# Performance work log

Measured on AMD Instinct MI355X. Metric: run time of the kernel, lower is better.

Reference implementation:

```python
import jax, jax.numpy as jnp
import numpy as np

D_MODEL, H, D_FF = 512, 8, 2048
DK = D_MODEL // H
EPS = 1e-5  # torch LayerNorm default


def layer_norm(x, g, b):
    m = jnp.mean(x, axis=-1, keepdims=True)
    v = jnp.mean((x - m) ** 2, axis=-1, keepdims=True)
    return (x - m) * jax.lax.rsqrt(v + EPS) * g + b


def setup_inputs() -> dict:
    key = jax.random.key(0)
    ks = jax.random.split(key, 10)
    B, S = 8, 2048
    s = lambda fan_in: 1.0 / np.sqrt(fan_in)
    return {
        "x": jax.random.normal(ks[0], (B, S, D_MODEL), jnp.float32),
        # per-head projections stacked: [h, d_model, dk] (bias-free Project)
        "wq": jax.random.uniform(ks[1], (H, D_MODEL, DK), jnp.float32, -s(D_MODEL), s(D_MODEL)),
        "wk": jax.random.uniform(ks[2], (H, D_MODEL, DK), jnp.float32, -s(D_MODEL), s(D_MODEL)),
        "wv": jax.random.uniform(ks[3], (H, D_MODEL, DK), jnp.float32, -s(D_MODEL), s(D_MODEL)),
        "wo": jax.random.uniform(ks[4], (D_MODEL, D_MODEL), jnp.float32, -s(D_MODEL), s(D_MODEL)),
        "w1": jax.random.uniform(ks[5], (D_MODEL, D_FF), jnp.float32, -s(D_MODEL), s(D_MODEL)),
        "b1": jax.random.uniform(ks[6], (D_FF,), jnp.float32, -s(D_MODEL), s(D_MODEL)),
        "w2": jax.random.uniform(ks[7], (D_FF, D_MODEL), jnp.float32, -s(D_FF), s(D_FF)),
        "b2": jax.random.uniform(ks[8], (D_MODEL,), jnp.float32, -s(D_FF), s(D_FF)),
        "ln1_g": jnp.ones((D_MODEL,), jnp.float32),
        "ln1_b": jnp.zeros((D_MODEL,), jnp.float32),
        "ln2_g": jnp.ones((D_MODEL,), jnp.float32),
        "ln2_b": jnp.zeros((D_MODEL,), jnp.float32),
    }


def reference(x, wq, wk, wv, wo, w1, b1, w2, b2, ln1_g, ln1_b, ln2_g, ln2_b):
    B, S, D = x.shape
    # --- multi-head self-attention (8 per-head Linears fused into one einsum) ---
    q = jnp.einsum("bsd,hdk->bhsk", x, wq)
    k = jnp.einsum("bsd,hdk->bhsk", x, wk)
    v = jnp.einsum("bsd,hdk->bhsk", x, wv)
    score = jnp.einsum("bhsk,bhtk->bhst", q, k) * (1.0 / np.sqrt(DK))
    attn = jax.nn.softmax(score, axis=-1)
    heads = jnp.einsum("bhst,bhtk->bhsk", attn, v)
    concat = heads.transpose(0, 2, 1, 3).reshape(B, S, D)  # cat over heads
    mha = concat @ wo
    # dropout in eval mode -> identity
    x = layer_norm(mha + x, ln1_g, ln1_b)
    # --- feed-forward ---
    ffn = jax.nn.relu(x @ w1 + b1) @ w2 + b2
    return layer_norm(ffn + x, ln2_g, ln2_b)
```

## Files before the change

### kernel.cpp

```cpp
#include <hip/hip_runtime.h>
#include <hip/hip_bf16.h>
#include <math.h>


#define D_MODEL 512
#define NHEAD   8
#define DKH     64
#define SEQ     2048
#define BATCH   8
#define DFF     2048
#define MROWS   (BATCH * SEQ)
#define QKVLD   1536

typedef __bf16 bf16x8 __attribute__((ext_vector_type(8)));
typedef float  f32x4  __attribute__((ext_vector_type(4)));

__device__ __forceinline__ unsigned short f2bf(float f) {
    union { float f; unsigned u; } v; v.f = f;
    return (unsigned short)((v.u + 0x7FFFu + ((v.u >> 16) & 1u)) >> 16);
}

__device__ __forceinline__ float bf2f(unsigned short u) {
    union { unsigned u; float f; } v; v.u = (unsigned)u << 16;
    return v.f;
}

__device__ __forceinline__ unsigned cvtpk(float a, float b) {
    unsigned r;
    asm("v_cvt_pk_bf16_f32 %0, %1, %2" : "=v"(r) : "v"(a), "v"(b));
    return r;
}

__device__ __forceinline__ float fexp2(float x) {
    float r; asm("v_exp_f32 %0, %1" : "=v"(r) : "v"(x)); return r;
}

__device__ __forceinline__ f32x4 mfma16(bf16x8 a, bf16x8 b, f32x4 c) {
    return __builtin_amdgcn_mfma_f32_16x16x32_bf16(a, b, c, 0, 0, 0);
}

__device__ __forceinline__ void gld_lds16(const unsigned short* g, unsigned short* l) {
    __builtin_amdgcn_global_load_lds(
        (const __attribute__((address_space(1))) unsigned int*)g,
        (__attribute__((address_space(3))) unsigned int*)l, 16, 0, 0);
}

template<bool BIAS, bool RELU, int RESMODE, bool OUTF32>
__global__ __launch_bounds__(256)
void mfma_gemm(const unsigned short* __restrict__ Av,
               const unsigned short* __restrict__ Bt,
               const float* __restrict__ bias, const void* __restrict__ resv,
               void* __restrict__ Cv, int Kdim, int lda, int ldc)
{
    __shared__ unsigned short As[2][128][32];
    __shared__ unsigned short Bs[2][128][32];

    const int tid  = threadIdx.x;
    const int lane = tid & 63;
    const int w    = tid >> 6;
    const int mq   = (w >> 1) << 6;
    const int nq   = (w & 1) << 6;
    const int lrow = lane & 15;
    const int g    = lane >> 4;
    const int lk   = g << 3;

    const int row0 = blockIdx.y << 7;
    const int col0 = blockIdx.x << 7;

    const int c0   = w << 5;
    const int srow = lane >> 2;
    const int scol = (lane & 3) << 3;
    const size_t aoff = (size_t)(row0 + c0 + srow) * lda  + scol;
    const size_t boff = (size_t)(col0 + c0 + srow) * Kdim + scol;

    auto stage = [&](int buf, int kt) {
        gld_lds16(Av + aoff + kt,                        &As[buf][c0     ][0]);
        gld_lds16(Av + aoff + (size_t)16 * lda  + kt,    &As[buf][c0 + 16][0]);
        gld_lds16(Bt + boff + kt,                        &Bs[buf][c0     ][0]);
        gld_lds16(Bt + boff + (size_t)16 * Kdim + kt,    &Bs[buf][c0 + 16][0]);
    };

    const f32x4 zero = {0.f, 0.f, 0.f, 0.f};
    f32x4 acc[4][4];
    #pragma unroll
    for (int i = 0; i < 4; ++i)
        #pragma unroll
        for (int j = 0; j < 4; ++j) acc[i][j] = zero;

    stage(0, 0);
    __syncthreads();

    int cur = 0;
    for (int kt = 0; kt < Kdim; kt += 32) {
        if (kt + 32 < Kdim) stage(cur ^ 1, kt + 32);

        bf16x8 af[4], bfv[4];
        #pragma unroll
        for (int mf = 0; mf < 4; ++mf)
            af[mf] = *(const bf16x8*)&As[cur][mq + mf * 16 + lrow][lk];
        #pragma unroll
        for (int nf = 0; nf < 4; ++nf)
            bfv[nf] = *(const bf16x8*)&Bs[cur][nq + nf * 16 + lrow][lk];
        #pragma unroll
        for (int mf = 0; mf < 4; ++mf)
            #pragma unroll
            for (int nf = 0; nf < 4; ++nf)
                acc[mf][nf] = mfma16(af[mf], bfv[nf], acc[mf][nf]);

        __syncthreads();
        cur ^= 1;
    }

    const int orow = row0 + mq + g * 4;
    const int ocol = col0 + nq + lrow;
    #pragma unroll
    for (int mf = 0; mf < 4; ++mf) {
        #pragma unroll
        for (int nf = 0; nf < 4; ++nf) {
            const int cc = ocol + nf * 16;
            float bv = 0.f;
            if constexpr (BIAS) bv = bias[cc];
            float v[4];
            #pragma unroll
            for (int r = 0; r < 4; ++r) {
                const int rr = orow + mf * 16 + r;
                v[r] = acc[mf][nf][r];
                if constexpr (BIAS) v[r] += bv;
                if constexpr (RELU) v[r] = fmaxf(v[r], 0.f);
                if constexpr (RESMODE == 1)
                    v[r] += ((const float*)resv)[(size_t)rr * ldc + cc];
                if constexpr (RESMODE == 2)
                    v[r] += bf2f(((const unsigned short*)resv)[(size_t)rr * ldc + cc]);
                if constexpr (OUTF32) ((float*)Cv)[(size_t)rr * ldc + cc] = v[r];
            }
            if constexpr (!OUTF32) {
                const unsigned u01 = cvtpk(v[0], v[1]);
                const unsigned u23 = cvtpk(v[2], v[3]);
                unsigned short* cp = (unsigned short*)Cv + (size_t)(orow + mf * 16) * ldc + cc;
                cp[0]                 = (unsigned short)u01;
                cp[(size_t)ldc]       = (unsigned short)(u01 >> 16);
                cp[(size_t)ldc * 2]   = (unsigned short)u23;
                cp[(size_t)ldc * 3]   = (unsigned short)(u23 >> 16);
            }
        }
    }
}

__device__ __forceinline__ void softmax_store(
    f32x4* sacc, float* mrun, float* lpart, f32x4* oacc,
    unsigned short (*Ps)[76], int rowbase, int g, int lrow)
{
    float pmax[4];
    bool need = false;
    #pragma unroll
    for (int r = 0; r < 4; ++r) {
        pmax[r] = fmaxf(fmaxf(sacc[0][r], sacc[1][r]),
                        fmaxf(sacc[2][r], sacc[3][r]));
        need |= (pmax[r] > mrun[r] + 8.f);
    }
    if (__any(need)) {
        #pragma unroll
        for (int r = 0; r < 4; ++r) {
            float mt = pmax[r];
            mt = fmaxf(mt, __shfl_xor(mt, 1, 16));
            mt = fmaxf(mt, __shfl_xor(mt, 2, 16));
            mt = fmaxf(mt, __shfl_xor(mt, 4, 16));
            mt = fmaxf(mt, __shfl_xor(mt, 8, 16));
            const float mnew = fmaxf(mrun[r], mt);
            const float alpha = fexp2(mrun[r] - mnew);
            mrun[r] = mnew;
            lpart[r] *= alpha;
            #pragma unroll
            for (int nf = 0; nf < 4; ++nf) oacc[nf][r] *= alpha;
        }
    }
    #pragma unroll
    for (int r = 0; r < 4; ++r) {
        const float p0 = fexp2(sacc[0][r] - mrun[r]);
        const float p1 = fexp2(sacc[1][r] - mrun[r]);
        const float p2 = fexp2(sacc[2][r] - mrun[r]);
        const float p3 = fexp2(sacc[3][r] - mrun[r]);
        lpart[r] += (p0 + p1) + (p2 + p3);
        uint2 u;
        u.x = cvtpk(p0, p1);
        u.y = cvtpk(p2, p3);
        *(uint2*)&Ps[rowbase + g * 4 + r][4 * lrow] = u;
    }
}

__global__ __launch_bounds__(512, 4)
void mfma_attn(unsigned short* __restrict__ qkv)
{
    __shared__ unsigned short Ks[2][64][72];
    __shared__ unsigned short Vt[2][64][72];
    __shared__ unsigned short Ps[256][76];

    const int tid  = threadIdx.x;
    const int lane = tid & 63;
    const int w    = tid >> 6;
    const int lrow = lane & 15;
    const int g    = lane >> 4;
    const int lk   = g << 3;

    const int bid  = blockIdx.x;
    const int idx  = bid >> 3;
    const int bh   = (bid & 7) * 8 + (idx & 7);
    const int b  = bh >> 3, h = bh & 7;
    const int s0 = (idx >> 3) << 8;

    unsigned short* qptr = qkv + ((size_t)(b * SEQ + s0)) * QKVLD + h * DKH;
    const unsigned short* kbase = qkv + ((size_t)(b * SEQ)) * QKVLD + 512 + h * DKH;
    const unsigned short* vbase = qkv + ((size_t)(b * SEQ)) * QKVLD + 1024 + h * DKH;

    bf16x8 qf[2][2];
    #pragma unroll
    for (int sub = 0; sub < 2; ++sub) {
        const unsigned short* qp = qptr + (size_t)(w * 32 + sub * 16 + lrow) * QKVLD;
        qf[sub][0] = *(const bf16x8*)(qp + lk);
        qf[sub][1] = *(const bf16x8*)(qp + 32 + lk);
    }

    const int kr = tid >> 3, kc = (tid & 7) << 3;
    const int vr = tid & 63, vc = (tid >> 6) << 3;
    const int cvr = ((vr & 15) << 2) | (vr >> 4);

    uint4 kreg, vreg;
    auto loadKV = [&](int t0) {
        kreg = *(const uint4*)(kbase + (size_t)(t0 + kr) * QKVLD + kc);
        vreg = *(const uint4*)(vbase + (size_t)(t0 + vr) * QKVLD + vc);
    };
    loadKV(0);

    const f32x4 zero = {0.f, 0.f, 0.f, 0.f};
    f32x4 oacc0[4], oacc1[4];
    float m0[4], l0[4], m1[4], l1[4];
    #pragma unroll
    for (int i = 0; i < 4; ++i) {
        oacc0[i] = zero; oacc1[i] = zero;
        m0[i] = -INFINITY; m1[i] = -INFINITY; l0[i] = 0.f; l1[i] = 0.f;
    }

    for (int t0 = 0; t0 < SEQ; t0 += 64) {
        const int cur = (t0 >> 6) & 1;
        *(uint4*)&Ks[cur][kr][kc] = kreg;
        {
            const unsigned short* vu = (const unsigned short*)&vreg;
            #pragma unroll
            for (int j = 0; j < 8; ++j) Vt[cur][vc + j][cvr] = vu[j];
        }
        __syncthreads();

        if (t0 + 64 < SEQ) loadKV(t0 + 64);

        f32x4 s0a[4], s1a[4];
        #pragma unroll
        for (int nf = 0; nf < 4; ++nf) { s0a[nf] = zero; s1a[nf] = zero; }
        __builtin_amdgcn_s_setprio(1);
        #pragma unroll
        for (int kk = 0; kk < 2; ++kk) {
            #pragma unroll
            for (int nf = 0; nf < 4; ++nf) {
                const bf16x8 kf = *(const bf16x8*)&Ks[cur][nf * 16 + lrow][kk * 32 + lk];
                s0a[nf] = mfma16(qf[0][kk], kf, s0a[nf]);
                s1a[nf] = mfma16(qf[1][kk], kf, s1a[nf]);
            }
        }
        __builtin_amdgcn_s_setprio(0);

        softmax_store(s0a, m0, l0, oacc0, Ps, w * 32,      g, lrow);
        softmax_store(s1a, m1, l1, oacc1, Ps, w * 32 + 16, g, lrow);

        __builtin_amdgcn_s_setprio(1);
        #pragma unroll
        for (int kk = 0; kk < 2; ++kk) {
            const bf16x8 pf0 = *(const bf16x8*)&Ps[w * 32 + lrow][kk * 32 + lk];
            const bf16x8 pf1 = *(const bf16x8*)&Ps[w * 32 + 16 + lrow][kk * 32 + lk];
            #pragma unroll
            for (int nf = 0; nf < 4; ++nf) {
                const bf16x8 vf = *(const bf16x8*)&Vt[cur][nf * 16 + lrow][kk * 32 + lk];
                oacc0[nf] = mfma16(pf0, vf, oacc0[nf]);
                oacc1[nf] = mfma16(pf1, vf, oacc1[nf]);
            }
        }
        __builtin_amdgcn_s_setprio(0);
    }

    #pragma unroll
    for (int r = 0; r < 4; ++r) {
        float l = l0[r];
        l += __shfl_xor(l, 1, 16);
        l += __shfl_xor(l, 2, 16);
        l += __shfl_xor(l, 4, 16);
        l += __shfl_xor(l, 8, 16);
        const float inv = 1.f / l;
        #pragma unroll
        for (int nf = 0; nf < 4; ++nf)
            qptr[(size_t)(w * 32 + g * 4 + r) * QKVLD + nf * 16 + lrow] =
                f2bf(oacc0[nf][r] * inv);
    }
    #pragma unroll
    for (int r = 0; r < 4; ++r) {
        float l = l1[r];
        l += __shfl_xor(l, 1, 16);
        l += __shfl_xor(l, 2, 16);
        l += __shfl_xor(l, 4, 16);
        l += __shfl_xor(l, 8, 16);
        const float inv = 1.f / l;
        #pragma unroll
        for (int nf = 0; nf < 4; ++nf)
            qptr[(size_t)(w * 32 + 16 + g * 4 + r) * QKVLD + nf * 16 + lrow] =
                f2bf(oacc1[nf][r] * inv);
    }
}

template<bool WF32, bool WB16>
__global__ __launch_bounds__(256)
void ln_kernel(const float* __restrict__ in, const float* __restrict__ gg,
               const float* __restrict__ bb, float* __restrict__ outf,
               unsigned short* __restrict__ outb)
{
    const int row = blockIdx.x * 4 + (threadIdx.x >> 6);
    const int lane = threadIdx.x & 63;
    const float* p = in + (size_t)row * D_MODEL;

    const float4 a = *(const float4*)(p + lane * 4);
    const float4 c = *(const float4*)(p + 256 + lane * 4);
    float sum = a.x + a.y + a.z + a.w + c.x + c.y + c.z + c.w;
    float sq  = a.x*a.x + a.y*a.y + a.z*a.z + a.w*a.w
              + c.x*c.x + c.y*c.y + c.z*c.z + c.w*c.w;
    #pragma unroll
    for (int msk = 1; msk < 64; msk <<= 1) {
        sum += __shfl_xor(sum, msk, 64);
        sq  += __shfl_xor(sq,  msk, 64);
    }
    const float mean = sum * (1.f / 512.f);
    const float var  = sq * (1.f / 512.f) - mean * mean;
    const float rs   = rsqrtf(var + 1e-5f);

    const float4 g0 = *(const float4*)(gg + lane * 4);
    const float4 g1 = *(const float4*)(gg + 256 + lane * 4);
    const float4 b0 = *(const float4*)(bb + lane * 4);
    const float4 b1 = *(const float4*)(bb + 256 + lane * 4);

    float4 o0, o1;
    o0.x = (a.x - mean) * rs * g0.x + b0.x;
    o0.y = (a.y - mean) * rs * g0.y + b0.y;
    o0.z = (a.z - mean) * rs * g0.z + b0.z;
    o0.w = (a.w - mean) * rs * g0.w + b0.w;
    o1.x = (c.x - mean) * rs * g1.x + b1.x;
    o1.y = (c.y - mean) * rs * g1.y + b1.y;
    o1.z = (c.z - mean) * rs * g1.z + b1.z;
    o1.w = (c.w - mean) * rs * g1.w + b1.w;
    if constexpr (WF32) {
        *(float4*)(outf + (size_t)row * D_MODEL + lane * 4) = o0;
        *(float4*)(outf + (size_t)row * D_MODEL + 256 + lane * 4) = o1;
    }
    if constexpr (WB16) {
        uint2 pa, pb;
        pa.x = cvtpk(o0.x, o0.y);
        pa.y = cvtpk(o0.z, o0.w);
        pb.x = cvtpk(o1.x, o1.y);
        pb.y = cvtpk(o1.z, o1.w);
        *(uint2*)(outb + (size_t)row * D_MODEL + lane * 4) = pa;
        *(uint2*)(outb + (size_t)row * D_MODEL + 256 + lane * 4) = pb;
    }
}

__global__ __launch_bounds__(256)
void cast_bf16(const float* __restrict__ in, unsigned short* __restrict__ out)
{
    const size_t i = ((size_t)blockIdx.x * 256 + threadIdx.x) * 8;
    const float4 a = *(const float4*)(in + i);
    const float4 b = *(const float4*)(in + i + 4);
    uint4 o;
    o.x = cvtpk(a.x, a.y);
    o.y = cvtpk(a.z, a.w);
    o.z = cvtpk(b.x, b.y);
    o.w = cvtpk(b.z, b.w);
    *(uint4*)(out + i) = o;
}

__global__ __launch_bounds__(256)
void pack_qkv(const float* __restrict__ wq, const float* __restrict__ wk,
              const float* __restrict__ wv, unsigned short* __restrict__ Wqkv)
{
    const int idx = blockIdx.x * 256 + threadIdx.x;
    const int n = idx >> 9, d = idx & 511;
    const int h = n >> 6, c = n & 63;
    const size_t src = ((size_t)h * 512 + d) * 64 + c;
    Wqkv[idx]                 = f2bf(wq[src] * 0.18033688f);
    Wqkv[idx + 512 * 512]     = f2bf(wk[src]);
    Wqkv[idx + 2 * 512 * 512] = f2bf(wv[src]);
}

__global__ __launch_bounds__(256)
void pack_t(const float* __restrict__ in, unsigned short* __restrict__ out,
            int K, int N)
{
    __shared__ float t[32][33];
    const int kb = blockIdx.x << 5, nb = blockIdx.y << 5;
    const int c = threadIdx.x & 31, r0 = threadIdx.x >> 5;
    #pragma unroll
    for (int j = 0; j < 32; j += 8)
        t[r0 + j][c] = in[(size_t)(kb + r0 + j) * N + nb + c];
    __syncthreads();
    #pragma unroll
    for (int j = 0; j < 32; j += 8)
        out[(size_t)(nb + r0 + j) * K + kb + c] = f2bf(t[c][r0 + j]);
}

extern "C" void kernel_launch(void* const* d_in, const int* in_sizes, int n_in,
                              void* d_out, int out_size, void* d_ws, size_t ws_size,
                              hipStream_t stream)
{
    (void)in_sizes; (void)n_in; (void)out_size;

    const float* x    = (const float*)d_in[0];
    const float* wq   = (const float*)d_in[1];
    const float* wk   = (const float*)d_in[2];
    const float* wv   = (const float*)d_in[3];
    const float* wo   = (const float*)d_in[4];
    const float* w1   = (const float*)d_in[5];
    const float* b1   = (const float*)d_in[6];
    const float* w2   = (const float*)d_in[7];
    const float* b2   = (const float*)d_in[8];
    const float* ln1g = (const float*)d_in[9];
    const float* ln1b = (const float*)d_in[10];
    const float* ln2g = (const float*)d_in[11];
    const float* ln2b = (const float*)d_in[12];
    float* out = (float*)d_out;

    const size_t QKV_BYTES = (size_t)MROWS * QKVLD * 2;
    const size_t Y_BYTES   = (size_t)MROWS * D_MODEL * 4;
    unsigned char* base = (unsigned char*)d_ws;
    unsigned short* qkv  = (unsigned short*)(base);
    float*          y    = (float*)(base + QKV_BYTES);
    unsigned short* Wqkv = (unsigned short*)(base + QKV_BYTES + Y_BYTES);
    unsigned short* wo_t = Wqkv + 3 * 512 * 512;
    unsigned short* w1_t = wo_t + 512 * 512;
    unsigned short* w2_t = w1_t + 2048 * 512;
    unsigned short* hid  = w2_t + 2048 * 512;

    const size_t hid_off = (size_t)((unsigned char*)hid - base);
    const size_t avail = (ws_size > hid_off) ? (ws_size - hid_off) : 0;
    int chunk = (int)(avail / ((size_t)DFF * 2));
    chunk &= ~127;
    if (chunk > MROWS) chunk = MROWS;
    if (chunk < 128)   chunk = 128;

    float* y2 = (float*)qkv;
    unsigned short* xb  = (unsigned short*)d_out;
    unsigned short* x1b = (unsigned short*)d_out;

    pack_qkv<<<1024, 256, 0, stream>>>(wq, wk, wv, Wqkv);
    pack_t<<<dim3(16, 16), 256, 0, stream>>>(wo, wo_t, 512, 512);
    pack_t<<<dim3(16, 64), 256, 0, stream>>>(w1, w1_t, 512, 2048);
    pack_t<<<dim3(64, 16), 256, 0, stream>>>(w2, w2_t, 2048, 512);
    cast_bf16<<<(MROWS * D_MODEL) / (256 * 8), 256, 0, stream>>>(x, xb);

    const dim3 blk(256);

    mfma_gemm<false, false, 0, false>
        <<<dim3(12, MROWS / 128), blk, 0, stream>>>(xb, Wqkv, nullptr, nullptr,
                                                    qkv, 512, 512, QKVLD);

    mfma_attn<<<dim3(512), dim3(512), 0, stream>>>(qkv);

    mfma_gemm<false, false, 1, true>
        <<<dim3(4, MROWS / 128), blk, 0, stream>>>(qkv, wo_t, nullptr, x, y,
                                                   512, QKVLD, 512);

    ln_kernel<false, true><<<MROWS / 4, blk, 0, stream>>>(y, ln1g, ln1b,
                                                          nullptr, x1b);

    for (int r0 = 0; r0 < MROWS; r0 += chunk) {
        const int rows = (r0 + chunk <= MROWS) ? chunk : (MROWS - r0);
        mfma_gemm<true, true, 0, false>
            <<<dim3(DFF / 128, rows / 128), blk, 0, stream>>>(
                x1b + (size_t)r0 * D_MODEL, w1_t, b1, nullptr, hid,
                512, 512, DFF);
        mfma_gemm<true, false, 2, true>
            <<<dim3(4, rows / 128), blk, 0, stream>>>(
                hid, w2_t, b2, x1b + (size_t)r0 * D_MODEL,
                y2 + (size_t)r0 * D_MODEL, DFF, DFF, 512);
    }

    ln_kernel<true, false><<<MROWS / 4, blk, 0, stream>>>(y2, ln2g, ln2b,
                                                          out, nullptr);
}
```

Baseline: 294.8 us.

## Rewrite attention with 32x32 MFMA transposed scores and register-resident P via permlane swaps

```diff
diff --git a/kernel.cpp b/kernel.cpp
--- a/kernel.cpp
+++ b/kernel.cpp
@@ -14,6 +14,7 @@
 
 typedef __bf16 bf16x8 __attribute__((ext_vector_type(8)));
 typedef float  f32x4  __attribute__((ext_vector_type(4)));
+typedef float  f32x16 __attribute__((ext_vector_type(16)));
 
 __device__ __forceinline__ unsigned short f2bf(float f) {
     union { float f; unsigned u; } v; v.f = f;
@@ -35,8 +36,22 @@
     float r; asm("v_exp_f32 %0, %1" : "=v"(r) : "v"(x)); return r;
 }
 
+__device__ __forceinline__ void plswap(unsigned& x, unsigned& y) {
+    asm volatile("v_permlane32_swap_b32 %0, %1" : "+v"(x), "+v"(y));
+}
+
+__device__ __forceinline__ unsigned fbits(float f) {
+    union { float f; unsigned u; } v; v.f = f; return v.u;
+}
+__device__ __forceinline__ float bitsf(unsigned u) {
+    union { unsigned u; float f; } v; v.u = u; return v.f;
+}
+
 __device__ __forceinline__ f32x4 mfma16(bf16x8 a, bf16x8 b, f32x4 c) {
     return __builtin_amdgcn_mfma_f32_16x16x32_bf16(a, b, c, 0, 0, 0);
+}
+__device__ __forceinline__ f32x16 mfma32(bf16x8 a, bf16x8 b, f32x16 c) {
+    return __builtin_amdgcn_mfma_f32_32x32x16_bf16(a, b, c, 0, 0, 0);
 }
 
 __device__ __forceinline__ void gld_lds16(const unsigned short* g, unsigned short* l) {
@@ -146,83 +161,38 @@
     }
 }
 
-__device__ __forceinline__ void softmax_store(
-    f32x4* sacc, float* mrun, float* lpart, f32x4* oacc,
-    unsigned short (*Ps)[76], int rowbase, int g, int lrow)
-{
-    float pmax[4];
-    bool need = false;
-    #pragma unroll
-    for (int r = 0; r < 4; ++r) {
-        pmax[r] = fmaxf(fmaxf(sacc[0][r], sacc[1][r]),
-                        fmaxf(sacc[2][r], sacc[3][r]));
-        need |= (pmax[r] > mrun[r] + 8.f);
-    }
-    if (__any(need)) {
-        #pragma unroll
-        for (int r = 0; r < 4; ++r) {
-            float mt = pmax[r];
-            mt = fmaxf(mt, __shfl_xor(mt, 1, 16));
-            mt = fmaxf(mt, __shfl_xor(mt, 2, 16));
-            mt = fmaxf(mt, __shfl_xor(mt, 4, 16));
-            mt = fmaxf(mt, __shfl_xor(mt, 8, 16));
-            const float mnew = fmaxf(mrun[r], mt);
-            const float alpha = fexp2(mrun[r] - mnew);
-            mrun[r] = mnew;
-            lpart[r] *= alpha;
-            #pragma unroll
-            for (int nf = 0; nf < 4; ++nf) oacc[nf][r] *= alpha;
-        }
-    }
-    #pragma unroll
-    for (int r = 0; r < 4; ++r) {
-        const float p0 = fexp2(sacc[0][r] - mrun[r]);
-        const float p1 = fexp2(sacc[1][r] - mrun[r]);
-        const float p2 = fexp2(sacc[2][r] - mrun[r]);
-        const float p3 = fexp2(sacc[3][r] - mrun[r]);
-        lpart[r] += (p0 + p1) + (p2 + p3);
-        uint2 u;
-        u.x = cvtpk(p0, p1);
-        u.y = cvtpk(p2, p3);
-        *(uint2*)&Ps[rowbase + g * 4 + r][4 * lrow] = u;
-    }
-}
-
 __global__ __launch_bounds__(512, 4)
 void mfma_attn(unsigned short* __restrict__ qkv)
 {
     __shared__ unsigned short Ks[2][64][72];
     __shared__ unsigned short Vt[2][64][72];
-    __shared__ unsigned short Ps[256][76];
 
     const int tid  = threadIdx.x;
     const int lane = tid & 63;
     const int w    = tid >> 6;
-    const int lrow = lane & 15;
-    const int g    = lane >> 4;
-    const int lk   = g << 3;
+    const int q32  = lane & 31;
+    const int h    = lane >> 5;
 
     const int bid  = blockIdx.x;
     const int idx  = bid >> 3;
     const int bh   = (bid & 7) * 8 + (idx & 7);
-    const int b  = bh >> 3, h = bh & 7;
+    const int b  = bh >> 3, hd = bh & 7;
     const int s0 = (idx >> 3) << 8;
 
-    unsigned short* qptr = qkv + ((size_t)(b * SEQ + s0)) * QKVLD + h * DKH;
-    const unsigned short* kbase = qkv + ((size_t)(b * SEQ)) * QKVLD + 512 + h * DKH;
-    const unsigned short* vbase = qkv + ((size_t)(b * SEQ)) * QKVLD + 1024 + h * DKH;
-
-    bf16x8 qf[2][2];
-    #pragma unroll
-    for (int sub = 0; sub < 2; ++sub) {
-        const unsigned short* qp = qptr + (size_t)(w * 32 + sub * 16 + lrow) * QKVLD;
-        qf[sub][0] = *(const bf16x8*)(qp + lk);
-        qf[sub][1] = *(const bf16x8*)(qp + 32 + lk);
+    unsigned short* qptr = qkv + ((size_t)(b * SEQ + s0)) * QKVLD + hd * DKH;
+    const unsigned short* kbase = qkv + ((size_t)(b * SEQ)) * QKVLD + 512 + hd * DKH;
+    const unsigned short* vbase = qkv + ((size_t)(b * SEQ)) * QKVLD + 1024 + hd * DKH;
+
+    bf16x8 qf[4];
+    {
+        const unsigned short* qp = qptr + (size_t)(w * 32 + q32) * QKVLD + 8 * h;
+        #pragma unroll
+        for (int t = 0; t < 4; ++t)
+            qf[t] = *(const bf16x8*)(qp + 16 * t);
     }
 
     const int kr = tid >> 3, kc = (tid & 7) << 3;
     const int vr = tid & 63, vc = (tid >> 6) << 3;
-    const int cvr = ((vr & 15) << 2) | (vr >> 4);
 
     uint4 kreg, vreg;
     auto loadKV = [&](int t0) {
@@ -231,14 +201,10 @@
     };
     loadKV(0);
 
-    const f32x4 zero = {0.f, 0.f, 0.f, 0.f};
-    f32x4 oacc0[4], oacc1[4];
-    float m0[4], l0[4], m1[4], l1[4];
-    #pragma unroll
-    for (int i = 0; i < 4; ++i) {
-        oacc0[i] = zero; oacc1[i] = zero;
-        m0[i] = -INFINITY; m1[i] = -INFINITY; l0[i] = 0.f; l1[i] = 0.f;
-    }
+    f32x16 oacc0, oacc1;
+    #pragma unroll
+    for (int i = 0; i < 16; ++i) { oacc0[i] = 0.f; oacc1[i] = 0.f; }
+    float m = -INFINITY, lsum = 0.f;
 
     for (int t0 = 0; t0 < SEQ; t0 += 64) {
         const int cur = (t0 >> 6) & 1;
@@ -246,70 +212,99 @@
         {
             const unsigned short* vu = (const unsigned short*)&vreg;
             #pragma unroll
-            for (int j = 0; j < 8; ++j) Vt[cur][vc + j][cvr] = vu[j];
+            for (int j = 0; j < 8; ++j) Vt[cur][vc + j][vr] = vu[j];
         }
         __syncthreads();
 
         if (t0 + 64 < SEQ) loadKV(t0 + 64);
 
-        f32x4 s0a[4], s1a[4];
-        #pragma unroll
-        for (int nf = 0; nf < 4; ++nf) { s0a[nf] = zero; s1a[nf] = zero; }
+        f32x16 sa0, sa1;
+        #pragma unroll
+        for (int i = 0; i < 16; ++i) { sa0[i] = 0.f; sa1[i] = 0.f; }
         __builtin_amdgcn_s_setprio(1);
         #pragma unroll
-        for (int kk = 0; kk < 2; ++kk) {
+        for (int t = 0; t < 4; ++t) {
+            const bf16x8 k0 = *(const bf16x8*)&Ks[cur][q32     ][16 * t + 8 * h];
+            const bf16x8 k1 = *(const bf16x8*)&Ks[cur][32 + q32][16 * t + 8 * h];
+            sa0 = mfma32(k0, qf[t], sa0);
+            sa1 = mfma32(k1, qf[t], sa1);
+        }
+        __builtin_amdgcn_s_setprio(0);
+
+        float pmax = fmaxf(sa0[0], sa1[0]);
+        #pragma unroll
+        for (int r = 1; r < 16; ++r)
+            pmax = fmaxf(pmax, fmaxf(sa0[r], sa1[r]));
+        {
+            unsigned x = fbits(pmax), y = x;
+            plswap(x, y);
+            const float partner = (lane < 32) ? bitsf(y) : bitsf(x);
+            pmax = fmaxf(pmax, partner);
+        }
+        if (__any(pmax > m + 8.f)) {
+            const float mnew = fmaxf(m, pmax);
+            const float alpha = fexp2(m - mnew);
+            m = mnew;
+            lsum *= alpha;
             #pragma unroll
-            for (int nf = 0; nf < 4; ++nf) {
-                const bf16x8 kf = *(const bf16x8*)&Ks[cur][nf * 16 + lrow][kk * 32 + lk];
-                s0a[nf] = mfma16(qf[0][kk], kf, s0a[nf]);
-                s1a[nf] = mfma16(qf[1][kk], kf, s1a[nf]);
+            for (int r = 0; r < 16; ++r) {
+                const int qr = (r & 3) + 8 * (r >> 2) + 4 * h;
+                const float ar = __shfl(alpha, qr, 64);
+                oacc0[r] *= ar;
+                oacc1[r] *= ar;
             }
         }
+        #pragma unroll
+        for (int r = 0; r < 16; ++r) {
+            sa0[r] = fexp2(sa0[r] - m);
+            sa1[r] = fexp2(sa1[r] - m);
+            lsum += sa0[r] + sa1[r];
+        }
+
+        bf16x8 pa[4];
+        #pragma unroll
+        for (int blk = 0; blk < 2; ++blk) {
+            const f32x16& p = blk ? sa1 : sa0;
+            #pragma unroll
+            for (int tt = 0; tt < 2; ++tt) {
+                unsigned a0 = cvtpk(p[8 * tt + 0], p[8 * tt + 1]);
+                unsigned a1 = cvtpk(p[8 * tt + 2], p[8 * tt + 3]);
+                unsigned b0 = cvtpk(p[8 * tt + 4], p[8 * tt + 5]);
+                unsigned b1 = cvtpk(p[8 * tt + 6], p[8 * tt + 7]);
+                plswap(a0, b0);
+                plswap(a1, b1);
+                union { uint4 u; bf16x8 v; } cvt;
+                cvt.u.x = a0; cvt.u.y = a1; cvt.u.z = b0; cvt.u.w = b1;
+                pa[blk * 2 + tt] = cvt.v;
+            }
+        }
+
+        __builtin_amdgcn_s_setprio(1);
+        #pragma unroll
+        for (int ttg = 0; ttg < 4; ++ttg) {
+            const bf16x8 vf0 = *(const bf16x8*)&Vt[cur][q32     ][16 * ttg + 8 * h];
+            const bf16x8 vf1 = *(const bf16x8*)&Vt[cur][32 + q32][16 * ttg + 8 * h];
+            oacc0 = mfma32(pa[ttg], vf0, oacc0);
+            oacc1 = mfma32(pa[ttg], vf1, oacc1);
+        }
         __builtin_amdgcn_s_setprio(0);
-
-        softmax_store(s0a, m0, l0, oacc0, Ps, w * 32,      g, lrow);
-        softmax_store(s1a, m1, l1, oacc1, Ps, w * 32 + 16, g, lrow);
-
-        __builtin_amdgcn_s_setprio(1);
-        #pragma unroll
-        for (int kk = 0; kk < 2; ++kk) {
-            const bf16x8 pf0 = *(const bf16x8*)&Ps[w * 32 + lrow][kk * 32 + lk];
-            const bf16x8 pf1 = *(const bf16x8*)&Ps[w * 32 + 16 + lrow][kk * 32 + lk];
-            #pragma unroll
-            for (int nf = 0; nf < 4; ++nf) {
-                const bf16x8 vf = *(const bf16x8*)&Vt[cur][nf * 16 + lrow][kk * 32 + lk];
-                oacc0[nf] = mfma16(pf0, vf, oacc0[nf]);
-                oacc1[nf] = mfma16(pf1, vf, oacc1[nf]);
-            }
-        }
-        __builtin_amdgcn_s_setprio(0);
-    }
-
-    #pragma unroll
-    for (int r = 0; r < 4; ++r) {
-        float l = l0[r];
-        l += __shfl_xor(l, 1, 16);
-        l += __shfl_xor(l, 2, 16);
-        l += __shfl_xor(l, 4, 16);
-        l += __shfl_xor(l, 8, 16);
-        const float inv = 1.f / l;
-        #pragma unroll
-        for (int nf = 0; nf < 4; ++nf)
-            qptr[(size_t)(w * 32 + g * 4 + r) * QKVLD + nf * 16 + lrow] =
-                f2bf(oacc0[nf][r] * inv);
-    }
-    #pragma unroll
-    for (int r = 0; r < 4; ++r) {
-        float l = l1[r];
-        l += __shfl_xor(l, 1, 16);
-        l += __shfl_xor(l, 2, 16);
-        l += __shfl_xor(l, 4, 16);
-        l += __shfl_xor(l, 8, 16);
-        const float inv = 1.f / l;
-        #pragma unroll
-        for (int nf = 0; nf < 4; ++nf)
-            qptr[(size_t)(w * 32 + 16 + g * 4 + r) * QKVLD + nf * 16 + lrow] =
-                f2bf(oacc1[nf][r] * inv);
+    }
+
+    float ltot;
+    {
+        unsigned x = fbits(lsum), y = x;
+        plswap(x, y);
+        const float partner = (lane < 32) ? bitsf(y) : bitsf(x);
+        ltot = lsum + partner;
+    }
+    const float inv = 1.f / ltot;
+    #pragma unroll
+    for (int r = 0; r < 16; ++r) {
+        const int qr = (r & 3) + 8 * (r >> 2) + 4 * h;
+        const float invr = __shfl(inv, qr, 64);
+        unsigned short* op = qptr + (size_t)(w * 32 + qr) * QKVLD + q32;
+        op[0]  = f2bf(oacc0[r] * invr);
+        op[32] = f2bf(oacc1[r] * invr);
     }
 }
 
```

After: 292.2 us. No clear change (-0.9%).
